# Performance work log

Hardware: AMD Instinct MI355X
Metric: run time of the kernel (lower is better)

## Reference

```python
import jax, jax.numpy as jnp
import numpy as np

E = 8            # num_experts
DIM = 2880       # model dim
HID = 2880       # expert hidden dim (mlp1 outputs 2*HID, interleaved glu/linear)
T = 16384        # total dispatched tokens, evenly split across experts
SWIGLU_LIMIT = 7.0
ALPHA = 1.702


def swiglu(x, alpha=ALPHA, limit=SWIGLU_LIMIT):
    # interleaved: even channels -> glu gate, odd channels -> linear
    x_glu = x[..., ::2]
    x_lin = x[..., 1::2]
    x_glu = jnp.minimum(x_glu, limit)
    x_lin = jnp.clip(x_lin, -limit, limit)
    return x_glu * jax.nn.sigmoid(alpha * x_glu) * (x_lin + 1.0)


def setup_inputs() -> dict:
    key = jax.random.key(0)
    k1, k2, k3, k4, k5 = jax.random.split(key, 5)
    scale = 0.02
    x = jax.random.normal(k1, (T, DIM), dtype=jnp.float32)
    num_tokens_per_expert = jnp.full((E,), T // E, dtype=jnp.int64)
    mlp1_weight = jax.random.normal(k2, (E, 2 * HID, DIM), dtype=jnp.float32) * scale
    mlp1_bias = jax.random.normal(k3, (E, 2 * HID), dtype=jnp.float32) * scale
    mlp2_weight = jax.random.normal(k4, (E, DIM, HID), dtype=jnp.float32) * scale
    mlp2_bias = jax.random.normal(k5, (E, DIM), dtype=jnp.float32) * scale
    return {
        "x": x,
        "num_tokens_per_expert": num_tokens_per_expert,
        "mlp1_weight": mlp1_weight,
        "mlp1_bias": mlp1_bias,
        "mlp2_weight": mlp2_weight,
        "mlp2_bias": mlp2_bias,
    }


def reference(x, num_tokens_per_expert, mlp1_weight, mlp1_bias, mlp2_weight, mlp2_bias):
    # Equal token counts per expert (as constructed): grouped GEMM == batched GEMM
    # over a reshaped [E, T/E, DIM] view. tp_degree == 1 so ScaleBiasForward is identity.
    tpe = T // E
    xg = x.reshape(E, tpe, DIM)                                  # [E, t, D]
    h = jnp.einsum("etd,ehd->eth", xg, mlp1_weight)              # [E, t, 2H]
    h = h + mlp1_bias[:, None, :]
    h = swiglu(h)                                                # [E, t, H]
    out = jnp.einsum("eth,edh->etd", h, mlp2_weight)             # [E, t, D]
    out = out + mlp2_bias[:, None, :]
    return out.reshape(T, DIM)
```

## Files before the change

kernel.cpp:

```cpp
#include <hip/hip_runtime.h>
#include <hip/hip_bf16.h>


#define TT   16384
#define DIM_ 2880
#define HID_ 2880
#define NE   8
#define TPE  2048
#define KDIM 2880
#define NT   45

typedef __attribute__((ext_vector_type(8))) short short8;
typedef __attribute__((ext_vector_type(4))) float f32x4;

__device__ __forceinline__ unsigned short f2bf(float f) {
  unsigned u = __builtin_bit_cast(unsigned, f);
  u += 0x7fffu + ((u >> 16) & 1u);
  return (unsigned short)(u >> 16);
}

__global__ void __launch_bounds__(256) cvt_f32_bf16(const float* __restrict__ src,
                                                    unsigned short* __restrict__ dst,
                                                    long n) {
  long i = ((long)blockIdx.x * 256 + threadIdx.x) * 8;
  if (i >= n) return;
  float4 a = *(const float4*)(src + i);
  float4 b = *(const float4*)(src + i + 4);
  union { unsigned short u[8]; short8 v; } r;
  r.u[0] = f2bf(a.x); r.u[1] = f2bf(a.y); r.u[2] = f2bf(a.z); r.u[3] = f2bf(a.w);
  r.u[4] = f2bf(b.x); r.u[5] = f2bf(b.y); r.u[6] = f2bf(b.z); r.u[7] = f2bf(b.w);
  *(short8*)(dst + i) = r.v;
}

template<bool FUSE_SWIGLU>
__global__ void __launch_bounds__(512, 2) gemm4p(const unsigned short* __restrict__ A,
                                                 const unsigned short* __restrict__ B,
                                                 const float* __restrict__ bias,
                                                 void* __restrict__ Cout,
                                                 int M, int N) {
  __shared__ unsigned short As[2][256 * 64];
  __shared__ unsigned short Bs[2][320 * 64];

  const int tid  = threadIdx.x;
  const int lane = tid & 63;
  const int wid  = tid >> 6;
  const int wr   = wid >> 2;
  const int wc   = wid & 3;
  const int e    = blockIdx.z;

  const int ntn   = N / 320;
  const int ntm   = M / 256;
  const int per_e = ntn * ntm;
  const int bid   = blockIdx.x;
  const int swz   = (bid & 7) * (per_e >> 3) + (bid >> 3);
  const int m0    = (swz / ntn) * 256;
  const int n0    = (swz % ntn) * 320;

  const int srow = tid >> 3;
  const int scol = ((tid & 7) ^ (srow & 7)) << 3;
  const unsigned short* Aexp = A + ((size_t)e * M + m0 + srow) * KDIM + scol;
  const unsigned short* Bexp = B + ((size_t)e * N + n0 + srow) * KDIM + scol;

  auto stage = [&](int buf, int kt) {
    const unsigned short* asrc = Aexp + (size_t)kt * 64;
#pragma unroll
    for (int j = 0; j < 4; ++j)
      __builtin_amdgcn_global_load_lds(
          (const __attribute__((address_space(1))) unsigned int*)(asrc + (size_t)(j * 64) * KDIM),
          (__attribute__((address_space(3))) unsigned int*)(&As[buf][j * 4096 + tid * 8]),
          16, 0, 0);
    const unsigned short* bsrc = Bexp + (size_t)kt * 64;
#pragma unroll
    for (int j = 0; j < 5; ++j)
      __builtin_amdgcn_global_load_lds(
          (const __attribute__((address_space(1))) unsigned int*)(bsrc + (size_t)(j * 64) * KDIM),
          (__attribute__((address_space(3))) unsigned int*)(&Bs[buf][j * 4096 + tid * 8]),
          16, 0, 0);
  };

  const int arow = (wr * 128 + (lane & 15)) * 128;
  const int brow = (wc * 80  + (lane & 15)) * 128;
  const int swzb = (lane & 7) << 4;
  const int kb   = ((lane >> 4) & 3) * 16;
  const int c0 = kb ^ swzb;
  const int c1 = (64 + kb) ^ swzb;

  f32x4 acc[8][5] = {};

  stage(0, 0);
  stage(1, 1);
  asm volatile("s_waitcnt vmcnt(9)" ::: "memory");
  __builtin_amdgcn_s_barrier();

  for (int t = 0; t < NT; ++t) {
    const int cur = t & 1;
    const char* aB = (const char*)(&As[cur][0]) + arow;
    const char* bB = (const char*)(&Bs[cur][0]) + brow;

    short8 a[4], a2[4], b0[5], b1[5];

#pragma unroll
    for (int i = 0; i < 4; ++i) a[i] = *(const short8*)(aB + i * 2048 + c0);
#pragma unroll
    for (int f = 0; f < 5; ++f) b0[f] = *(const short8*)(bB + f * 2048 + c0);
    __builtin_amdgcn_s_barrier();
    asm volatile("s_waitcnt lgkmcnt(0)" ::: "memory");
    __builtin_amdgcn_s_setprio(1);
#pragma unroll
    for (int f = 0; f < 5; ++f)
#pragma unroll
      for (int i = 0; i < 4; ++i)
        acc[i][f] = __builtin_amdgcn_mfma_f32_16x16x32_bf16(a[i], b0[f], acc[i][f], 0, 0, 0);
    __builtin_amdgcn_s_setprio(0);
    __builtin_amdgcn_s_barrier();

#pragma unroll
    for (int i = 0; i < 4; ++i) a[i] = *(const short8*)(aB + (4 + i) * 2048 + c0);
    __builtin_amdgcn_s_barrier();
    asm volatile("s_waitcnt lgkmcnt(0)" ::: "memory");
    __builtin_amdgcn_s_setprio(1);
#pragma unroll
    for (int f = 0; f < 5; ++f)
#pragma unroll
      for (int i = 0; i < 4; ++i)
        acc[4 + i][f] = __builtin_amdgcn_mfma_f32_16x16x32_bf16(a[i], b0[f], acc[4 + i][f], 0, 0, 0);
    __builtin_amdgcn_s_setprio(0);
    __builtin_amdgcn_s_barrier();

#pragma unroll
    for (int i = 0; i < 4; ++i) a[i]  = *(const short8*)(aB + i * 2048 + c1);
#pragma unroll
    for (int f = 0; f < 5; ++f) b1[f] = *(const short8*)(bB + f * 2048 + c1);
#pragma unroll
    for (int i = 0; i < 4; ++i) a2[i] = *(const short8*)(aB + (4 + i) * 2048 + c1);
    __builtin_amdgcn_s_barrier();
    asm volatile("s_waitcnt lgkmcnt(0)" ::: "memory");
    __builtin_amdgcn_s_setprio(1);
#pragma unroll
    for (int f = 0; f < 5; ++f)
#pragma unroll
      for (int i = 0; i < 4; ++i)
        acc[i][f] = __builtin_amdgcn_mfma_f32_16x16x32_bf16(a[i], b1[f], acc[i][f], 0, 0, 0);
    __builtin_amdgcn_s_setprio(0);
    __builtin_amdgcn_s_barrier();

    const bool more = (t + 2 < NT);
    if (more) stage(cur, t + 2);
    __builtin_amdgcn_s_setprio(1);
#pragma unroll
    for (int f = 0; f < 5; ++f)
#pragma unroll
      for (int i = 0; i < 4; ++i)
        acc[4 + i][f] = __builtin_amdgcn_mfma_f32_16x16x32_bf16(a2[i], b1[f], acc[4 + i][f], 0, 0, 0);
    __builtin_amdgcn_s_setprio(0);
    if (more) asm volatile("s_waitcnt vmcnt(9)" ::: "memory");
    else      asm volatile("s_waitcnt vmcnt(0)" ::: "memory");
    __builtin_amdgcn_s_barrier();
  }

  const float* be = bias + (size_t)e * N;
  if constexpr (FUSE_SWIGLU) {
    unsigned short* ha = (unsigned short*)Cout + (size_t)e * M * (N >> 1);
#pragma unroll
    for (int fm = 0; fm < 8; ++fm)
#pragma unroll
      for (int fn = 0; fn < 5; ++fn) {
        const int col = n0 + wc * 80 + fn * 16 + (lane & 15);
        const float bc = be[col];
#pragma unroll
        for (int j = 0; j < 4; ++j) {
          const int row = m0 + wr * 128 + fm * 16 + (lane >> 4) * 4 + j;
          float v = acc[fm][fn][j] + bc;
          float p = __shfl_xor(v, 1);
          if (!(lane & 1)) {
            float g  = fminf(v, 7.0f);
            float l2 = fminf(fmaxf(p, -7.0f), 7.0f);
            float act = g / (1.0f + __expf(-1.702f * g)) * (l2 + 1.0f);
            ha[(size_t)row * (N >> 1) + (col >> 1)] = f2bf(act);
          }
        }
      }
  } else {
    float* out = (float*)Cout + (size_t)e * M * N;
#pragma unroll
    for (int fm = 0; fm < 8; ++fm)
#pragma unroll
      for (int fn = 0; fn < 5; ++fn) {
        const int col = n0 + wc * 80 + fn * 16 + (lane & 15);
        const float bc = be[col];
#pragma unroll
        for (int j = 0; j < 4; ++j) {
          const int row = m0 + wr * 128 + fm * 16 + (lane >> 4) * 4 + j;
          out[(size_t)row * N + col] = acc[fm][fn][j] + bc;
        }
      }
  }
}

extern "C" void kernel_launch(void* const* d_in, const int* in_sizes, int n_in,
                              void* d_out, int out_size, void* d_ws, size_t ws_size,
                              hipStream_t stream) {
  const float* x  = (const float*)d_in[0];
  const float* w1 = (const float*)d_in[2];
  const float* b1 = (const float*)d_in[3];
  const float* w2 = (const float*)d_in[4];
  const float* b2 = (const float*)d_in[5];

  unsigned short* xb  = (unsigned short*)d_ws;
  unsigned short* w1b = xb  + (size_t)TT * DIM_;
  unsigned short* w2b = w1b + (size_t)NE * 2 * HID_ * DIM_;
  unsigned short* ha  = w2b + (size_t)NE * DIM_ * HID_;

  const long nx = (long)TT * DIM_;
  const long n1 = (long)NE * 2 * HID_ * DIM_;
  const long n2 = (long)NE * DIM_ * HID_;
  cvt_f32_bf16<<<(int)(nx / 2048), 256, 0, stream>>>(x,  xb,  nx);
  cvt_f32_bf16<<<(int)(n1 / 2048), 256, 0, stream>>>(w1, w1b, n1);
  cvt_f32_bf16<<<(int)(n2 / 2048), 256, 0, stream>>>(w2, w2b, n2);

  dim3 g1((5760 / 320) * (TPE / 256), 1, NE);
  gemm4p<true><<<g1, 512, 0, stream>>>(xb, w1b, b1, ha, TPE, 5760);

  dim3 g2((DIM_ / 320) * (TPE / 256), 1, NE);
  gemm4p<false><<<g2, 512, 0, stream>>>(ha, w2b, b2, (float*)d_out, TPE, DIM_);
}
```

Before: 1.381 ms.

## Shrink GEMM N-tile to 192 and interleave staged loads across four MFMA phases

Reduces the B tile from 320 to 192 columns per block, which lowers accumulator registers and LDS use and raises block count. It also splits the next-tile global-to-LDS staging into chunks issued during separate MFMA phases, reorders the phases to k-half then m-half, and waits with vmcnt(2) instead of draining. The goal is to overlap memory traffic with compute more evenly and improve occupancy, at the cost of lower arithmetic intensity per block and more A-tile reloads across N tiles.

```diff
diff --git a/kernel.cpp b/kernel.cpp
--- a/kernel.cpp
+++ b/kernel.cpp
@@ -32,14 +32,19 @@
   *(short8*)(dst + i) = r.v;
 }
 
+#define GLDS(gsrc, ldst) \
+  __builtin_amdgcn_global_load_lds( \
+      (const __attribute__((address_space(1))) unsigned int*)(gsrc), \
+      (__attribute__((address_space(3))) unsigned int*)(ldst), 16, 0, 0)
+
 template<bool FUSE_SWIGLU>
-__global__ void __launch_bounds__(512, 2) gemm4p(const unsigned short* __restrict__ A,
+__global__ void __launch_bounds__(512, 2) gemm8p(const unsigned short* __restrict__ A,
                                                  const unsigned short* __restrict__ B,
                                                  const float* __restrict__ bias,
                                                  void* __restrict__ Cout,
                                                  int M, int N) {
   __shared__ unsigned short As[2][256 * 64];
-  __shared__ unsigned short Bs[2][320 * 64];
+  __shared__ unsigned short Bs[2][192 * 64];
 
   const int tid  = threadIdx.x;
   const int lane = tid & 63;
@@ -48,66 +53,64 @@
   const int wc   = wid & 3;
   const int e    = blockIdx.z;
 
-  const int ntn   = N / 320;
+  const int ntn   = N / 192;
   const int ntm   = M / 256;
   const int per_e = ntn * ntm;
   const int bid   = blockIdx.x;
   const int swz   = (bid & 7) * (per_e >> 3) + (bid >> 3);
   const int m0    = (swz / ntn) * 256;
-  const int n0    = (swz % ntn) * 320;
+  const int n0    = (swz % ntn) * 192;
 
   const int srow = tid >> 3;
   const int scol = ((tid & 7) ^ (srow & 7)) << 3;
   const unsigned short* Aexp = A + ((size_t)e * M + m0 + srow) * KDIM + scol;
   const unsigned short* Bexp = B + ((size_t)e * N + n0 + srow) * KDIM + scol;
 
-  auto stage = [&](int buf, int kt) {
-    const unsigned short* asrc = Aexp + (size_t)kt * 64;
-#pragma unroll
-    for (int j = 0; j < 4; ++j)
-      __builtin_amdgcn_global_load_lds(
-          (const __attribute__((address_space(1))) unsigned int*)(asrc + (size_t)(j * 64) * KDIM),
-          (__attribute__((address_space(3))) unsigned int*)(&As[buf][j * 4096 + tid * 8]),
-          16, 0, 0);
-    const unsigned short* bsrc = Bexp + (size_t)kt * 64;
-#pragma unroll
-    for (int j = 0; j < 5; ++j)
-      __builtin_amdgcn_global_load_lds(
-          (const __attribute__((address_space(1))) unsigned int*)(bsrc + (size_t)(j * 64) * KDIM),
-          (__attribute__((address_space(3))) unsigned int*)(&Bs[buf][j * 4096 + tid * 8]),
-          16, 0, 0);
+  auto stageA2 = [&](int buf, int kt, int ja, int jb) {
+    const unsigned short* src = Aexp + (size_t)kt * 64;
+    GLDS(src + (size_t)(ja * 64) * KDIM, &As[buf][ja * 4096 + tid * 8]);
+    GLDS(src + (size_t)(jb * 64) * KDIM, &As[buf][jb * 4096 + tid * 8]);
   };
+  auto stageB3 = [&](int buf, int kt) {
+    const unsigned short* src = Bexp + (size_t)kt * 64;
+#pragma unroll
+    for (int j = 0; j < 3; ++j)
+      GLDS(src + (size_t)(j * 64) * KDIM, &Bs[buf][j * 4096 + tid * 8]);
+  };
 
   const int arow = (wr * 128 + (lane & 15)) * 128;
-  const int brow = (wc * 80  + (lane & 15)) * 128;
+  const int brow = (wc * 48  + (lane & 15)) * 128;
   const int swzb = (lane & 7) << 4;
   const int kb   = ((lane >> 4) & 3) * 16;
   const int c0 = kb ^ swzb;
   const int c1 = (64 + kb) ^ swzb;
 
-  f32x4 acc[8][5] = {};
-
-  stage(0, 0);
-  stage(1, 1);
-  asm volatile("s_waitcnt vmcnt(9)" ::: "memory");
+  f32x4 acc[8][3] = {};
+  short8 a[4], b0[3], b1[3];
+
+  stageA2(0, 0, 0, 1); stageA2(0, 0, 2, 3);
+  stageB3(0, 0);
+  stageA2(1, 1, 0, 2);
+  asm volatile("s_waitcnt vmcnt(2)" ::: "memory");
   __builtin_amdgcn_s_barrier();
 
   for (int t = 0; t < NT; ++t) {
     const int cur = t & 1;
     const char* aB = (const char*)(&As[cur][0]) + arow;
     const char* bB = (const char*)(&Bs[cur][0]) + brow;
-
-    short8 a[4], a2[4], b0[5], b1[5];
-
-#pragma unroll
-    for (int i = 0; i < 4; ++i) a[i] = *(const short8*)(aB + i * 2048 + c0);
-#pragma unroll
-    for (int f = 0; f < 5; ++f) b0[f] = *(const short8*)(bB + f * 2048 + c0);
-    __builtin_amdgcn_s_barrier();
-    asm volatile("s_waitcnt lgkmcnt(0)" ::: "memory");
-    __builtin_amdgcn_s_setprio(1);
-#pragma unroll
-    for (int f = 0; f < 5; ++f)
+    const bool n1ok = (t + 1 < NT);
+    const bool n2ok = (t + 2 < NT);
+
+#pragma unroll
+    for (int i = 0; i < 4; ++i) a[i]  = *(const short8*)(aB + i * 2048 + c0);
+#pragma unroll
+    for (int f = 0; f < 3; ++f) b0[f] = *(const short8*)(bB + f * 2048 + c0);
+    if (n1ok) stageA2(cur ^ 1, t + 1, 1, 3);
+    __builtin_amdgcn_s_barrier();
+    asm volatile("s_waitcnt lgkmcnt(0)" ::: "memory");
+    __builtin_amdgcn_s_setprio(1);
+#pragma unroll
+    for (int f = 0; f < 3; ++f)
 #pragma unroll
       for (int i = 0; i < 4; ++i)
         acc[i][f] = __builtin_amdgcn_mfma_f32_16x16x32_bf16(a[i], b0[f], acc[i][f], 0, 0, 0);
@@ -115,12 +118,29 @@
     __builtin_amdgcn_s_barrier();
 
 #pragma unroll
+    for (int i = 0; i < 4; ++i) a[i]  = *(const short8*)(aB + i * 2048 + c1);
+#pragma unroll
+    for (int f = 0; f < 3; ++f) b1[f] = *(const short8*)(bB + f * 2048 + c1);
+    if (n1ok) stageB3(cur ^ 1, t + 1);
+    __builtin_amdgcn_s_barrier();
+    asm volatile("s_waitcnt lgkmcnt(0)" ::: "memory");
+    __builtin_amdgcn_s_setprio(1);
+#pragma unroll
+    for (int f = 0; f < 3; ++f)
+#pragma unroll
+      for (int i = 0; i < 4; ++i)
+        acc[i][f] = __builtin_amdgcn_mfma_f32_16x16x32_bf16(a[i], b1[f], acc[i][f], 0, 0, 0);
+    __builtin_amdgcn_s_setprio(0);
+    __builtin_amdgcn_s_barrier();
+
+#pragma unroll
     for (int i = 0; i < 4; ++i) a[i] = *(const short8*)(aB + (4 + i) * 2048 + c0);
-    __builtin_amdgcn_s_barrier();
-    asm volatile("s_waitcnt lgkmcnt(0)" ::: "memory");
-    __builtin_amdgcn_s_setprio(1);
-#pragma unroll
-    for (int f = 0; f < 5; ++f)
+    if (n2ok) stageA2(cur, t + 2, 0, 2);
+    __builtin_amdgcn_s_barrier();
+    asm volatile("s_waitcnt lgkmcnt(0)" ::: "memory");
+    __builtin_amdgcn_s_setprio(1);
+#pragma unroll
+    for (int f = 0; f < 3; ++f)
 #pragma unroll
       for (int i = 0; i < 4; ++i)
         acc[4 + i][f] = __builtin_amdgcn_mfma_f32_16x16x32_bf16(a[i], b0[f], acc[4 + i][f], 0, 0, 0);
@@ -128,32 +148,17 @@
     __builtin_amdgcn_s_barrier();
 
 #pragma unroll
-    for (int i = 0; i < 4; ++i) a[i]  = *(const short8*)(aB + i * 2048 + c1);
-#pragma unroll
-    for (int f = 0; f < 5; ++f) b1[f] = *(const short8*)(bB + f * 2048 + c1);
-#pragma unroll
-    for (int i = 0; i < 4; ++i) a2[i] = *(const short8*)(aB + (4 + i) * 2048 + c1);
-    __builtin_amdgcn_s_barrier();
-    asm volatile("s_waitcnt lgkmcnt(0)" ::: "memory");
-    __builtin_amdgcn_s_setprio(1);
-#pragma unroll
-    for (int f = 0; f < 5; ++f)
-#pragma unroll
-      for (int i = 0; i < 4; ++i)
-        acc[i][f] = __builtin_amdgcn_mfma_f32_16x16x32_bf16(a[i], b1[f], acc[i][f], 0, 0, 0);
-    __builtin_amdgcn_s_setprio(0);
-    __builtin_amdgcn_s_barrier();
-
-    const bool more = (t + 2 < NT);
-    if (more) stage(cur, t + 2);
-    __builtin_amdgcn_s_setprio(1);
-#pragma unroll
-    for (int f = 0; f < 5; ++f)
-#pragma unroll
-      for (int i = 0; i < 4; ++i)
-        acc[4 + i][f] = __builtin_amdgcn_mfma_f32_16x16x32_bf16(a2[i], b1[f], acc[4 + i][f], 0, 0, 0);
-    __builtin_amdgcn_s_setprio(0);
-    if (more) asm volatile("s_waitcnt vmcnt(9)" ::: "memory");
+    for (int i = 0; i < 4; ++i) a[i] = *(const short8*)(aB + (4 + i) * 2048 + c1);
+    __builtin_amdgcn_s_barrier();
+    asm volatile("s_waitcnt lgkmcnt(0)" ::: "memory");
+    __builtin_amdgcn_s_setprio(1);
+#pragma unroll
+    for (int f = 0; f < 3; ++f)
+#pragma unroll
+      for (int i = 0; i < 4; ++i)
+        acc[4 + i][f] = __builtin_amdgcn_mfma_f32_16x16x32_bf16(a[i], b1[f], acc[4 + i][f], 0, 0, 0);
+    __builtin_amdgcn_s_setprio(0);
+    if (n2ok) asm volatile("s_waitcnt vmcnt(2)" ::: "memory");
     else      asm volatile("s_waitcnt vmcnt(0)" ::: "memory");
     __builtin_amdgcn_s_barrier();
   }
@@ -164,8 +169,8 @@
 #pragma unroll
     for (int fm = 0; fm < 8; ++fm)
 #pragma unroll
-      for (int fn = 0; fn < 5; ++fn) {
-        const int col = n0 + wc * 80 + fn * 16 + (lane & 15);
+      for (int fn = 0; fn < 3; ++fn) {
+        const int col = n0 + wc * 48 + fn * 16 + (lane & 15);
         const float bc = be[col];
 #pragma unroll
         for (int j = 0; j < 4; ++j) {
@@ -185,8 +190,8 @@
 #pragma unroll
     for (int fm = 0; fm < 8; ++fm)
 #pragma unroll
-      for (int fn = 0; fn < 5; ++fn) {
-        const int col = n0 + wc * 80 + fn * 16 + (lane & 15);
+      for (int fn = 0; fn < 3; ++fn) {
+        const int col = n0 + wc * 48 + fn * 16 + (lane & 15);
         const float bc = be[col];
 #pragma unroll
         for (int j = 0; j < 4; ++j) {
@@ -218,9 +223,9 @@
   cvt_f32_bf16<<<(int)(n1 / 2048), 256, 0, stream>>>(w1, w1b, n1);
   cvt_f32_bf16<<<(int)(n2 / 2048), 256, 0, stream>>>(w2, w2b, n2);
 
-  dim3 g1((5760 / 320) * (TPE / 256), 1, NE);
-  gemm4p<true><<<g1, 512, 0, stream>>>(xb, w1b, b1, ha, TPE, 5760);
-
-  dim3 g2((DIM_ / 320) * (TPE / 256), 1, NE);
-  gemm4p<false><<<g2, 512, 0, stream>>>(ha, w2b, b2, (float*)d_out, TPE, DIM_);
-}
+  dim3 g1((5760 / 192) * (TPE / 256), 1, NE);
+  gemm8p<true><<<g1, 512, 0, stream>>>(xb, w1b, b1, ha, TPE, 5760);
+
+  dim3 g2((DIM_ / 192) * (TPE / 256), 1, NE);
+  gemm8p<false><<<g2, 512, 0, stream>>>(ha, w2b, b2, (float*)d_out, TPE, DIM_);
+}
```

Result: slower. 1.485 ms (+7.5%).
